# Performance work log

Hardware: AMD Instinct MI355X
Metric: run time of the kernel (lower is better)

## Reference

```python
import jax, jax.numpy as jnp
import numpy as np
from jax import lax

B, L, D, H, DH, NL, FF, V, CH = 64, 512, 384, 12, 32, 6, 1536, 30522, 64


def setup_inputs() -> dict:
    key = jax.random.key(0)
    ks = jax.random.split(key, 16)
    n = lambda i, shape, s: jax.random.normal(ks[i], shape, dtype=jnp.float32) * s
    return {
        "input_ids": jax.random.randint(ks[0], (B, L), 0, V),
        "attention_mask": jnp.ones((B, L), jnp.int32),
        "word_emb": n(1, (V, D), 0.02),
        "pos_emb": n(2, (L, D), 0.02),
        "type_emb": n(3, (2, D), 0.02),
        "emb_ln_w": jnp.ones((D,)), "emb_ln_b": jnp.zeros((D,)),
        "qW": n(4, (NL, D, D), 0.05), "kW": n(5, (NL, D, D), 0.05),
        "vW": n(6, (NL, D, D), 0.05), "oW": n(7, (NL, D, D), 0.05),
        "gW": n(8, (NL, D, D), 0.05),
        "convW": n(9, (NL, D, 1, 4), 0.1), "convB": jnp.zeros((NL, D)),
        "fdecay": jnp.full((NL, H, DH), 0.3, jnp.float32),
        "sdecay": jnp.full((NL, H, DH), 0.9, jnp.float32),
        "surW": n(10, (NL, 1, 2 * DH), 0.1), "surB": jnp.zeros((NL, 1)),
        "alpha": jnp.full((NL,), 0.5, jnp.float32),
        "ln1_w": jnp.ones((NL, D)), "ln1_b": jnp.zeros((NL, D)),
        "ffnW1": n(11, (NL, FF, D), 0.05), "ffnB1": jnp.zeros((NL, FF)),
        "ffnW2": n(12, (NL, D, FF), 0.05), "ffnB2": jnp.zeros((NL, D)),
        "ln2_w": jnp.ones((NL, D)), "ln2_b": jnp.zeros((NL, D)),
    }


def _ln(x, w, b, eps=1e-12):
    m = x.mean(-1, keepdims=True)
    v = ((x - m) ** 2).mean(-1, keepdims=True)
    return (x - m) * lax.rsqrt(v + eps) * w + b


def _delta(q, k, v, wfac):
    # chunked delta-rule linear attention: state[d,e] decays by wfac per chunk
    Bq, Hq, Lq, Dh = q.shape
    nC = Lq // CH
    chunk = lambda t: t.reshape(Bq, Hq, nC, CH, Dh).transpose(2, 0, 1, 3, 4)

    def step(state, xs):
        qc, kc, vc = xs
        state = state * wfac + jnp.einsum('bhld,bhle->bhde', vc, kc)
        return state, jnp.einsum('bhld,bhde->bhle', qc, state)

    s0 = jnp.zeros((Bq, Hq, Dh, Dh), q.dtype)
    _, o = lax.scan(step, s0, (chunk(q), chunk(k), chunk(v)))
    return o.transpose(1, 2, 0, 3, 4).reshape(Bq, Hq, Lq, Dh)


def _titan(x, qW, kW, vW, oW, gW, convW, convB, fdec, sdec, surW, surB, alpha):
    Bx, Lx, Dx = x.shape
    # depthwise conv1d, kernel=4, padding=2, truncate to L (torch semantics)
    xc = lax.conv_general_dilated(x.transpose(0, 2, 1), convW, (1,), [(2, 2)],
                                  feature_group_count=Dx,
                                  dimension_numbers=('NCH', 'OIH', 'NCH'))
    xc = (xc + convB[None, :, None])[:, :, :Lx].transpose(0, 2, 1)
    xc = jax.nn.silu(xc)
    proj = lambda W: (xc @ W.T).reshape(Bx, Lx, H, DH).transpose(0, 2, 1, 3)
    q, k, v = proj(qW), proj(kW), proj(vW)
    v = v * jax.nn.sigmoid(proj(gW))
    # surprise gate on concatenated (k, v)
    s = jax.nn.sigmoid((jnp.concatenate([k, v], -1) @ surW.T + surB) * 10.0)
    wfac_f = jnp.mean(jax.nn.sigmoid(fdec)) ** CH
    wfac_s = jnp.mean(jax.nn.sigmoid(sdec)) ** CH
    o_fast = _delta(q, k, v, wfac_f)
    o_slow = _delta(q, k * s, v * s, wfac_s)
    a = jax.nn.sigmoid(alpha)
    o = a * o_fast + (1.0 - a) * o_slow
    return o.transpose(0, 2, 1, 3).reshape(Bx, Lx, Dx) @ oW.T


def reference(input_ids, attention_mask, word_emb, pos_emb, type_emb, emb_ln_w,
              emb_ln_b, qW, kW, vW, oW, gW, convW, convB, fdecay, sdecay, surW,
              surB, alpha, ln1_w, ln1_b, ffnW1, ffnB1, ffnW2, ffnB2, ln2_w, ln2_b):
    x = word_emb[input_ids] + pos_emb[None, :L] + type_emb[0]
    x = _ln(x, emb_ln_w, emb_ln_b)
    for i in range(NL):
        attn = _titan(x, qW[i], kW[i], vW[i], oW[i], gW[i], convW[i], convB[i],
                      fdecay[i], sdecay[i], surW[i], surB[i], alpha[i])
        x = _ln(x + attn, ln1_w[i], ln1_b[i])
        h = jax.nn.gelu(x @ ffnW1[i].T + ffnB1[i], approximate=False)
        x = _ln(x + h @ ffnW2[i].T + ffnB2[i], ln2_w[i], ln2_b[i])
    m = attention_mask[..., None].astype(x.dtype)
    emb = (x * m).sum(1) / jnp.clip(m.sum(1), 1e-9)
    return emb / jnp.clip(jnp.linalg.norm(emb, axis=1, keepdims=True), 1e-12)
```

## Files before the change

### kernel.cpp

```cpp
#include <hip/hip_runtime.h>
#include <hip/hip_bf16.h>
#include <math.h>

constexpr int B_  = 64;
constexpr int L_  = 512;
constexpr int D_  = 384;
constexpr int H_  = 12;
constexpr int DH_ = 32;
constexpr int NL_ = 6;
constexpr int FF_ = 1536;
constexpr int CH_ = 64;
constexpr int MT  = B_ * L_;
constexpr int DD  = D_ * D_;

typedef float f32x4 __attribute__((ext_vector_type(4)));
typedef short s16x8 __attribute__((ext_vector_type(8)));
typedef short s16x4 __attribute__((ext_vector_type(4)));

__device__ __forceinline__ short f2bf(float f) {
    unsigned u = __float_as_uint(f);
    unsigned r = (u + 0x7fffu + ((u >> 16) & 1u)) >> 16;
    return (short)r;
}
__device__ __forceinline__ float bf2f(short s) {
    unsigned u = ((unsigned)(unsigned short)s) << 16;
    return __uint_as_float(u);
}

__global__ void cvt_kernel(const float* __restrict__ src, short* __restrict__ dst, int n8) {
    int i = blockIdx.x * 256 + threadIdx.x;
    if (i >= n8) return;
    const float4 lo = *(const float4*)(src + (size_t)i * 8);
    const float4 hi = *(const float4*)(src + (size_t)i * 8 + 4);
    s16x8 t;
    t[0] = f2bf(lo.x); t[1] = f2bf(lo.y); t[2] = f2bf(lo.z); t[3] = f2bf(lo.w);
    t[4] = f2bf(hi.x); t[5] = f2bf(hi.y); t[6] = f2bf(hi.z); t[7] = f2bf(hi.w);
    *(s16x8*)(dst + (size_t)i * 8) = t;
}

__global__ void cvt4_kernel(const float* __restrict__ q, const float* __restrict__ k,
                            const float* __restrict__ v, const float* __restrict__ g,
                            short* __restrict__ dst) {
    int i = blockIdx.x * 256 + threadIdx.x;
    if (i >= NL_ * DD / 8) return;
    const int l = i / (DD / 8), r = i - l * (DD / 8);
    const float* srcs[4] = {q, k, v, g};
#pragma unroll
    for (int w = 0; w < 4; w++) {
        const float4 lo = *(const float4*)(srcs[w] + (size_t)i * 8);
        const float4 hi = *(const float4*)(srcs[w] + (size_t)i * 8 + 4);
        s16x8 t;
        t[0] = f2bf(lo.x); t[1] = f2bf(lo.y); t[2] = f2bf(lo.z); t[3] = f2bf(lo.w);
        t[4] = f2bf(hi.x); t[5] = f2bf(hi.y); t[6] = f2bf(hi.z); t[7] = f2bf(hi.w);
        *(s16x8*)(dst + ((size_t)(l * 4 + w) * DD) + (size_t)r * 8) = t;
    }
}

__global__ __launch_bounds__(256) void embed_ln_kernel(
        const int* __restrict__ ids, const float* __restrict__ wemb,
        const float* __restrict__ pemb, const float* __restrict__ temb,
        const float* __restrict__ w, const float* __restrict__ b,
        float* __restrict__ out, short* __restrict__ outb) {
    const int t    = blockIdx.x * 4 + (threadIdx.x >> 6);
    const int lane = threadIdx.x & 63;
    const int l    = t % L_;
    const size_t ro = (size_t)t * D_;
    const size_t wo = (size_t)ids[t] * D_;
    const size_t po = (size_t)l * D_;

    float v[6];
    float s = 0.f;
#pragma unroll
    for (int j = 0; j < 6; j++) {
        const int d = j * 64 + lane;
        v[j] = wemb[wo + d] + pemb[po + d] + temb[d];
        s += v[j];
    }
#pragma unroll
    for (int o = 32; o > 0; o >>= 1) s += __shfl_xor(s, o);
    const float m = s * (1.f / D_);
    float s2 = 0.f;
#pragma unroll
    for (int j = 0; j < 6; j++) { v[j] -= m; s2 += v[j] * v[j]; }
#pragma unroll
    for (int o = 32; o > 0; o >>= 1) s2 += __shfl_xor(s2, o);
    const float r = rsqrtf(s2 * (1.f / D_) + 1e-12f);
#pragma unroll
    for (int j = 0; j < 6; j++) {
        const int d = j * 64 + lane;
        const float o = v[j] * r * w[d] + b[d];
        out[ro + d]  = o;
        outb[ro + d] = f2bf(o);
    }
}

__global__ __launch_bounds__(256) void ln_res_kernel(
        const short* __restrict__ y, float* __restrict__ x, short* __restrict__ xb,
        const float* __restrict__ w, const float* __restrict__ b) {
    const int t    = blockIdx.x * 4 + (threadIdx.x >> 6);
    const int lane = threadIdx.x & 63;
    const size_t ro = (size_t)t * D_;

    float v[6];
    float s = 0.f;
#pragma unroll
    for (int j = 0; j < 6; j++) {
        const int d = j * 64 + lane;
        v[j] = x[ro + d] + bf2f(y[ro + d]);
        s += v[j];
    }
#pragma unroll
    for (int o = 32; o > 0; o >>= 1) s += __shfl_xor(s, o);
    const float m = s * (1.f / D_);
    float s2 = 0.f;
#pragma unroll
    for (int j = 0; j < 6; j++) { v[j] -= m; s2 += v[j] * v[j]; }
#pragma unroll
    for (int o = 32; o > 0; o >>= 1) s2 += __shfl_xor(s2, o);
    const float r = rsqrtf(s2 * (1.f / D_) + 1e-12f);
#pragma unroll
    for (int j = 0; j < 6; j++) {
        const int d = j * 64 + lane;
        const float o = v[j] * r * w[d] + b[d];
        x[ro + d]  = o;
        xb[ro + d] = f2bf(o);
    }
}

__global__ void wfac_kernel(const float* __restrict__ fdec, const float* __restrict__ sdec,
                            float* __restrict__ wf) {
    const int l     = blockIdx.x >> 1;
    const int which = blockIdx.x & 1;
    const float* p  = (which ? sdec : fdec) + (size_t)l * H_ * DH_;
    float v = 1.f / (1.f + expf(-p[threadIdx.x]));
    __shared__ float red[6];
#pragma unroll
    for (int o = 32; o > 0; o >>= 1) v += __shfl_down(v, o);
    if ((threadIdx.x & 63) == 0) red[threadIdx.x >> 6] = v;
    __syncthreads();
    if (threadIdx.x == 0) {
        float s = 0.f;
        for (int i = 0; i < 6; i++) s += red[i];
        float m = s / (float)(H_ * DH_);
        for (int i = 0; i < 6; i++) m = m * m;
        wf[l * 2 + which] = m;
    }
}

__global__ __launch_bounds__(256) void conv_silu_kernel(
        const short* __restrict__ xb, const float* __restrict__ cw,
        const float* __restrict__ cb, short* __restrict__ out) {
    const int i8 = blockIdx.x * 256 + threadIdx.x;
    const int d8 = (i8 * 8) % D_;
    const int bl = (i8 * 8) / D_;
    const int l  = bl % L_;

    float acc[8];
#pragma unroll
    for (int jj = 0; jj < 8; jj++) acc[jj] = cb[d8 + jj];

    const short* xrow = xb + (size_t)(bl - l) * D_ + d8;
#pragma unroll
    for (int j = 0; j < 4; j++) {
        const int t = l + j - 2;
        if (t >= 0 && t < L_) {
            const s16x8 xv = *(const s16x8*)(xrow + (size_t)t * D_);
#pragma unroll
            for (int jj = 0; jj < 8; jj++)
                acc[jj] = fmaf(bf2f(xv[jj]), cw[(d8 + jj) * 4 + j], acc[jj]);
        }
    }
    s16x8 o;
#pragma unroll
    for (int jj = 0; jj < 8; jj++) {
        const float sv = acc[jj] / (1.f + expf(-acc[jj]));
        o[jj] = f2bf(sv);
    }
    *(s16x8*)(out + (size_t)i8 * 8) = o;
}

template <int ACT, bool BIAS>
__global__ __launch_bounds__(256) void gemm_mfma(const short* __restrict__ A_b,
                                                 const short* __restrict__ Wb,
                                                 const float* __restrict__ bias,
                                                 short* __restrict__ Cb0,
                                                 int N, int K, int zsW, int zsC) {
    const short* W = Wb + (size_t)blockIdx.z * zsW;

    __shared__ short As[2][4096];
    __shared__ short Ws[2][4096];

    const int bm = blockIdx.y * 128, bn = blockIdx.x * 128;
    const int tid = threadIdx.x;
    const int wv = tid >> 6, lane = tid & 63;
    const int wr = wv >> 1, wc = wv & 1;
    const int l16 = lane & 15, kqr = lane >> 4;
    (void)wv; (void)lane;

    int srow[2], sq[2], sslot[2];
#pragma unroll
    for (int i = 0; i < 2; i++) {
        const int c = tid + i * 256;
        const int r = c >> 2;
        const int q = c & 3;
        srow[i]  = r;
        sq[i]    = q;
        sslot[i] = r * 4 + (q ^ ((r ^ (r >> 2)) & 3));
    }

    f32x4 acc[4][4];
    const f32x4 zr = {0.f, 0.f, 0.f, 0.f};
#pragma unroll
    for (int i = 0; i < 4; i++)
#pragma unroll
        for (int j = 0; j < 4; j++) acc[i][j] = zr;

    const int NT = K >> 5;
    s16x8 ra[2], rw[2];

#pragma unroll
    for (int i = 0; i < 2; i++) {
        ra[i] = *(const s16x8*)(A_b + (size_t)(bm + srow[i]) * K + sq[i] * 8);
        rw[i] = *(const s16x8*)(W   + (size_t)(bn + srow[i]) * K + sq[i] * 8);
    }
#pragma unroll
    for (int i = 0; i < 2; i++) {
        *(s16x8*)&As[0][sslot[i] * 8] = ra[i];
        *(s16x8*)&Ws[0][sslot[i] * 8] = rw[i];
    }
    __syncthreads();

    for (int kt = 0; kt < NT; ++kt) {
        const int buf = kt & 1;
        if (kt + 1 < NT) {
            const int ko = (kt + 1) * 32;
#pragma unroll
            for (int i = 0; i < 2; i++) {
                ra[i] = *(const s16x8*)(A_b + (size_t)(bm + srow[i]) * K + ko + sq[i] * 8);
                rw[i] = *(const s16x8*)(W   + (size_t)(bn + srow[i]) * K + ko + sq[i] * 8);
            }
        }

        s16x8 af[4], bf[4];
#pragma unroll
        for (int i = 0; i < 4; i++) {
            const int r = wr * 64 + i * 16 + l16;
            const int slot = r * 4 + (kqr ^ ((r ^ (r >> 2)) & 3));
            af[i] = *(const s16x8*)&As[buf][slot * 8];
        }
#pragma unroll
        for (int j = 0; j < 4; j++) {
            const int r = wc * 64 + j * 16 + l16;
            const int slot = r * 4 + (kqr ^ ((r ^ (r >> 2)) & 3));
            bf[j] = *(const s16x8*)&Ws[buf][slot * 8];
        }
#pragma unroll
        for (int i = 0; i < 4; i++)
#pragma unroll
            for (int j = 0; j < 4; j++)
                acc[i][j] = __builtin_amdgcn_mfma_f32_16x16x32_bf16(af[i], bf[j], acc[i][j], 0, 0, 0);

        if (kt + 1 < NT) {
            __syncthreads();
#pragma unroll
            for (int i = 0; i < 2; i++) {
                *(s16x8*)&As[buf ^ 1][sslot[i] * 8] = ra[i];
                *(s16x8*)&Ws[buf ^ 1][sslot[i] * 8] = rw[i];
            }
        }
        __syncthreads();
    }

    short* Cb = Cb0 + (size_t)blockIdx.z * zsC;
#pragma unroll
    for (int i = 0; i < 4; i++) {
        const int m0 = bm + wr * 64 + i * 16 + kqr * 4;
#pragma unroll
        for (int j = 0; j < 4; j++) {
            const int n = bn + wc * 64 + j * 16 + l16;
            float bv = 0.f;
            if (BIAS) bv = bias[n];
            const f32x4 v = acc[i][j];
#pragma unroll
            for (int r = 0; r < 4; r++) {
                float o = v[r] + bv;
                if (ACT == 1) o = 0.5f * o * (1.f + erff(o * 0.70710678118654752f));
                Cb[(size_t)(m0 + r) * N + n] = f2bf(o);
            }
        }
    }
}

__global__ __launch_bounds__(256) void delta_kernel(const short* __restrict__ qb,
                                                    const short* __restrict__ kb,
                                                    const short* __restrict__ vb,
                                                    const short* __restrict__ gb,
                                                    const float* __restrict__ surW,
                                                    const float* __restrict__ surB,
                                                    const float* __restrict__ wf,
                                                    const float* __restrict__ alpha,
                                                    int layer, short* __restrict__ ob) {
    const int bh = blockIdx.x;
    const int b = bh / H_, h = bh % H_;
    const int tid = threadIdx.x;
    const float wfa = wf[layer * 2 + 0], wsa = wf[layer * 2 + 1];
    const float a = 1.f / (1.f + expf(-alpha[layer]));
    const float sbias = surB[0];

    __shared__ float qS[CH_][36], kS[CH_][36], vS[CH_][36];
    __shared__ float s2S[CH_];
    __shared__ float Sc[DH_][36];
    __shared__ float swS[64];

    if (tid < 64) swS[tid] = surW[tid];
    __syncthreads();

    const int d  = tid >> 3;
    const int e4 = (tid & 7) * 4;
    const int lo = tid >> 2;
    const int e8 = (tid & 3) * 8;

    float sf[4] = {0.f, 0.f, 0.f, 0.f};
    float ss[4] = {0.f, 0.f, 0.f, 0.f};

    const size_t base = ((size_t)b * L_) * D_ + (size_t)h * DH_;

    for (int c = 0; c < L_ / CH_; c++) {
        const int l0 = c * CH_;
#pragma unroll
        for (int i = 0; i < 2; i++) {
            const int c4 = tid + i * 256;
            const int ll = c4 >> 3, dd4 = (c4 & 7) * 4;
            const size_t g = base + (size_t)(l0 + ll) * D_ + dd4;
            const s16x4 q4 = *(const s16x4*)(qb + g);
            const s16x4 k4 = *(const s16x4*)(kb + g);
            const s16x4 v4 = *(const s16x4*)(vb + g);
            const s16x4 g4 = *(const s16x4*)(gb + g);
            float p = 0.f;
#pragma unroll
            for (int j = 0; j < 4; j++) {
                const float kf = bf2f(k4[j]);
                const float gv = bf2f(g4[j]);
                const float vg = bf2f(v4[j]) / (1.f + expf(-gv));
                qS[ll][dd4 + j] = bf2f(q4[j]);
                kS[ll][dd4 + j] = kf;
                vS[ll][dd4 + j] = vg;
                p += kf * swS[dd4 + j] + vg * swS[32 + dd4 + j];
            }
            p += __shfl_xor(p, 1);
            p += __shfl_xor(p, 2);
            p += __shfl_xor(p, 4);
            if ((tid & 7) == 0) {
                const float sv = 1.f / (1.f + expf(-10.f * (p + sbias)));
                s2S[ll] = sv * sv;
            }
        }
        __syncthreads();

#pragma unroll
        for (int j = 0; j < 4; j++) { sf[j] *= wfa; ss[j] *= wsa; }
        for (int l = 0; l < CH_; l++) {
            const float vd = vS[l][d];
            const float s2 = s2S[l];
            const float4 k4 = *(const float4*)&kS[l][e4];
            const float kk[4] = {k4.x, k4.y, k4.z, k4.w};
#pragma unroll
            for (int j = 0; j < 4; j++) {
                const float p = vd * kk[j];
                sf[j] += p;
                ss[j] = fmaf(p, s2, ss[j]);
            }
        }
        float4 scv;
        scv.x = a * sf[0] + (1.f - a) * ss[0];
        scv.y = a * sf[1] + (1.f - a) * ss[1];
        scv.z = a * sf[2] + (1.f - a) * ss[2];
        scv.w = a * sf[3] + (1.f - a) * ss[3];
        *(float4*)&Sc[d][e4] = scv;
        __syncthreads();

        float o8[8] = {0.f, 0.f, 0.f, 0.f, 0.f, 0.f, 0.f, 0.f};
        for (int dd = 0; dd < DH_; dd++) {
            const float qv = qS[lo][dd];
            const float4 s0 = *(const float4*)&Sc[dd][e8];
            const float4 s1 = *(const float4*)&Sc[dd][e8 + 4];
            o8[0] = fmaf(qv, s0.x, o8[0]); o8[1] = fmaf(qv, s0.y, o8[1]);
            o8[2] = fmaf(qv, s0.z, o8[2]); o8[3] = fmaf(qv, s0.w, o8[3]);
            o8[4] = fmaf(qv, s1.x, o8[4]); o8[5] = fmaf(qv, s1.y, o8[5]);
            o8[6] = fmaf(qv, s1.z, o8[6]); o8[7] = fmaf(qv, s1.w, o8[7]);
        }
        s16x8 t;
#pragma unroll
        for (int j = 0; j < 8; j++) t[j] = f2bf(o8[j]);
        *(s16x8*)(ob + base + (size_t)(l0 + lo) * D_ + e8) = t;
        __syncthreads();
    }
}

__global__ __launch_bounds__(384) void pool_partial_kernel(
        const float* __restrict__ x, const int* __restrict__ mask,
        float* __restrict__ partial, float* __restrict__ maskp) {
    const int b  = blockIdx.x >> 3;
    const int ch = blockIdx.x & 7;
    const int dd = threadIdx.x;
    const int lb = ch * 64;
    float sum = 0.f;
    for (int l = 0; l < 64; l++) {
        const float m = (float)mask[b * L_ + lb + l];
        sum = fmaf(x[((size_t)(b * L_ + lb + l)) * D_ + dd], m, sum);
    }
    partial[(size_t)blockIdx.x * D_ + dd] = sum;
    if (dd < 64) {
        float mm = (float)mask[b * L_ + lb + dd];
#pragma unroll
        for (int o = 32; o > 0; o >>= 1) mm += __shfl_xor(mm, o);
        if (dd == 0) maskp[blockIdx.x] = mm;
    }
}

__global__ __launch_bounds__(384) void pool_finalize_kernel(
        const float* __restrict__ partial, const float* __restrict__ maskp,
        float* __restrict__ out) {
    const int b  = blockIdx.x;
    const int dd = threadIdx.x;
    float sum = 0.f, msum = 0.f;
#pragma unroll
    for (int c = 0; c < 8; c++) {
        sum  += partial[(size_t)(b * 8 + c) * D_ + dd];
        msum += maskp[b * 8 + c];
    }
    const float emb = sum / fmaxf(msum, 1e-9f);

    __shared__ float red[6];
    __shared__ float scale;
    float q = emb * emb;
#pragma unroll
    for (int o = 32; o > 0; o >>= 1) q += __shfl_down(q, o);
    if ((dd & 63) == 0) red[dd >> 6] = q;
    __syncthreads();
    if (dd == 0) {
        float t = 0.f;
        for (int i = 0; i < 6; i++) t += red[i];
        scale = 1.f / fmaxf(sqrtf(t), 1e-12f);
    }
    __syncthreads();
    out[(size_t)b * D_ + dd] = emb * scale;
}

extern "C" void kernel_launch(void* const* d_in, const int* in_sizes, int n_in,
                              void* d_out, int out_size, void* d_ws, size_t ws_size,
                              hipStream_t stream) {
    (void)in_sizes; (void)n_in; (void)out_size; (void)ws_size;

    const int*   ids   = (const int*)d_in[0];
    const int*   mask  = (const int*)d_in[1];
    const float* wemb  = (const float*)d_in[2];
    const float* pemb  = (const float*)d_in[3];
    const float* temb  = (const float*)d_in[4];
    const float* elnw  = (const float*)d_in[5];
    const float* elnb  = (const float*)d_in[6];
    const float* qW    = (const float*)d_in[7];
    const float* kW    = (const float*)d_in[8];
    const float* vW    = (const float*)d_in[9];
    const float* oW    = (const float*)d_in[10];
    const float* gW    = (const float*)d_in[11];
    const float* convW = (const float*)d_in[12];
    const float* convB = (const float*)d_in[13];
    const float* fdec  = (const float*)d_in[14];
    const float* sdec  = (const float*)d_in[15];
    const float* surW  = (const float*)d_in[16];
    const float* surB  = (const float*)d_in[17];
    const float* alpha = (const float*)d_in[18];
    const float* ln1w  = (const float*)d_in[19];
    const float* ln1b  = (const float*)d_in[20];
    const float* fW1   = (const float*)d_in[21];
    const float* fB1   = (const float*)d_in[22];
    const float* fW2   = (const float*)d_in[23];
    const float* fB2   = (const float*)d_in[24];
    const float* ln2w  = (const float*)d_in[25];
    const float* ln2b  = (const float*)d_in[26];

    float* x     = (float*)d_ws;
    float* wfp   = x + (size_t)MT * D_;
    float* pp    = wfp + 16;
    float* mp    = pp + (size_t)B_ * 8 * D_;
    short* qkvg  = (short*)(mp + B_ * 8);
    short* xb    = qkvg + (size_t)4 * MT * D_;
    short* xcb   = xb + (size_t)MT * D_;
    short* wqkvg = xcb + (size_t)MT * D_;
    short* wo    = wqkvg + (size_t)NL_ * 4 * DD;
    short* wf1   = wo + (size_t)NL_ * DD;
    short* wf2   = wf1 + (size_t)NL_ * FF_ * D_;

    short* q16 = qkvg;
    short* k16 = q16 + (size_t)MT * D_;
    short* v16 = k16 + (size_t)MT * D_;
    short* g16 = v16 + (size_t)MT * D_;
    short* attn = qkvg;
    short* hb   = qkvg;
    short* dob  = xcb;

    cvt4_kernel<<<NL_ * DD / 8 / 256, 256, 0, stream>>>(qW, kW, vW, gW, wqkvg);
    cvt_kernel<<<NL_ * DD / 8 / 256, 256, 0, stream>>>(oW, wo, NL_ * DD / 8);
    cvt_kernel<<<NL_ * FF_ * D_ / 8 / 256, 256, 0, stream>>>(fW1, wf1, NL_ * FF_ * D_ / 8);
    cvt_kernel<<<NL_ * FF_ * D_ / 8 / 256, 256, 0, stream>>>(fW2, wf2, NL_ * FF_ * D_ / 8);

    embed_ln_kernel<<<MT / 4, 256, 0, stream>>>(ids, wemb, pemb, temb, elnw, elnb, x, xb);
    wfac_kernel<<<NL_ * 2, 384, 0, stream>>>(fdec, sdec, wfp);

    const dim3 g1(D_ / 128, MT / 128, 1);
    const dim3 g2(FF_ / 128, MT / 128, 1);
    const dim3 gq(D_ / 128, MT / 128, 4);

    for (int i = 0; i < NL_; i++) {
        conv_silu_kernel<<<(MT * D_ / 8) / 256, 256, 0, stream>>>(
            xb, convW + (size_t)i * D_ * 4, convB + (size_t)i * D_, xcb);

        gemm_mfma<0, false><<<gq, 256, 0, stream>>>(
            xcb, wqkvg + (size_t)i * 4 * DD, nullptr, qkvg, D_, D_, DD, MT * D_);

        delta_kernel<<<B_ * H_, 256, 0, stream>>>(
            q16, k16, v16, g16, surW + (size_t)i * 2 * DH_, surB + i, wfp, alpha, i, dob);

        gemm_mfma<0, false><<<g1, 256, 0, stream>>>(
            dob, wo + (size_t)i * DD, nullptr, attn, D_, D_, 0, 0);
        ln_res_kernel<<<MT / 4, 256, 0, stream>>>(attn, x, xb, ln1w + (size_t)i * D_, ln1b + (size_t)i * D_);

        gemm_mfma<1, true><<<g2, 256, 0, stream>>>(
            xb, wf1 + (size_t)i * FF_ * D_, fB1 + (size_t)i * FF_, hb, FF_, D_, 0, 0);
        gemm_mfma<0, true><<<g1, 256, 0, stream>>>(
            hb, wf2 + (size_t)i * FF_ * D_, fB2 + (size_t)i * D_, xcb, D_, FF_, 0, 0);
        ln_res_kernel<<<MT / 4, 256, 0, stream>>>(xcb, x, xb, ln2w + (size_t)i * D_, ln2b + (size_t)i * D_);
    }

    pool_partial_kernel<<<B_ * 8, 384, 0, stream>>>(x, mask, pp, mp);
    pool_finalize_kernel<<<B_, 384, 0, stream>>>(pp, mp, (float*)d_out);
}
```

Measured before the change: 2.851 ms.

## Use direct global-to-LDS loads in GEMM and interleave QKVG output layout

The GEMM main loop now issues global_load_lds 16-byte transfers straight into the swizzled shared-memory buffers. This replaces the register staging and the extra barrier plus LDS store that came before. The Q/K/V/G projection becomes one GEMM with N=4*D writing a token-interleaved [MT,4D] buffer, and the delta kernel reads q/k/v/g from that layout at fixed offsets. The aim is to save register traffic and a sync per k-step. The cost is that the swizzled LDS slot mapping now depends on the wave/lane order of the direct-load writes, and the delta kernel's loads become strided across a wider row.

New measurement: 2.838 ms. Within noise of the previous version (-0.4%).

```diff
diff --git a/kernel.cpp b/kernel.cpp
--- a/kernel.cpp
+++ b/kernel.cpp
@@ -12,6 +12,7 @@
 constexpr int CH_ = 64;
 constexpr int MT  = B_ * L_;
 constexpr int DD  = D_ * D_;
+constexpr int TS  = 4 * D_;
 
 typedef float f32x4 __attribute__((ext_vector_type(4)));
 typedef short s16x8 __attribute__((ext_vector_type(8)));
@@ -25,6 +26,11 @@
 __device__ __forceinline__ float bf2f(short s) {
     unsigned u = ((unsigned)(unsigned short)s) << 16;
     return __uint_as_float(u);
+}
+
+__device__ __forceinline__ void gl_lds16(const void* g, void* l) {
+    __builtin_amdgcn_global_load_lds((const __attribute__((address_space(1))) void*)g,
+                                     (__attribute__((address_space(3))) void*)l, 16, 0, 0);
 }
 
 __global__ void cvt_kernel(const float* __restrict__ src, short* __restrict__ dst, int n8) {
@@ -181,12 +187,10 @@
 
 template <int ACT, bool BIAS>
 __global__ __launch_bounds__(256) void gemm_mfma(const short* __restrict__ A_b,
-                                                 const short* __restrict__ Wb,
+                                                 const short* __restrict__ W,
                                                  const float* __restrict__ bias,
-                                                 short* __restrict__ Cb0,
-                                                 int N, int K, int zsW, int zsC) {
-    const short* W = Wb + (size_t)blockIdx.z * zsW;
-
+                                                 short* __restrict__ Cb,
+                                                 int N, int K) {
     __shared__ short As[2][4096];
     __shared__ short Ws[2][4096];
 
@@ -195,17 +199,14 @@
     const int wv = tid >> 6, lane = tid & 63;
     const int wr = wv >> 1, wc = wv & 1;
     const int l16 = lane & 15, kqr = lane >> 4;
-    (void)wv; (void)lane;
-
-    int srow[2], sq[2], sslot[2];
+
+    int srow[2], skq[2];
 #pragma unroll
     for (int i = 0; i < 2; i++) {
         const int c = tid + i * 256;
         const int r = c >> 2;
-        const int q = c & 3;
-        srow[i]  = r;
-        sq[i]    = q;
-        sslot[i] = r * 4 + (q ^ ((r ^ (r >> 2)) & 3));
+        srow[i] = r;
+        skq[i] = (c & 3) ^ ((r ^ (r >> 2)) & 3);
     }
 
     f32x4 acc[4][4];
@@ -216,17 +217,13 @@
         for (int j = 0; j < 4; j++) acc[i][j] = zr;
 
     const int NT = K >> 5;
-    s16x8 ra[2], rw[2];
 
 #pragma unroll
     for (int i = 0; i < 2; i++) {
-        ra[i] = *(const s16x8*)(A_b + (size_t)(bm + srow[i]) * K + sq[i] * 8);
-        rw[i] = *(const s16x8*)(W   + (size_t)(bn + srow[i]) * K + sq[i] * 8);
-    }
-#pragma unroll
-    for (int i = 0; i < 2; i++) {
-        *(s16x8*)&As[0][sslot[i] * 8] = ra[i];
-        *(s16x8*)&Ws[0][sslot[i] * 8] = rw[i];
+        short* la = &As[0][(wv * 64 + i * 256) * 8];
+        short* lw = &Ws[0][(wv * 64 + i * 256) * 8];
+        gl_lds16(A_b + (size_t)(bm + srow[i]) * K + skq[i] * 8, la);
+        gl_lds16(W   + (size_t)(bn + srow[i]) * K + skq[i] * 8, lw);
     }
     __syncthreads();
 
@@ -236,8 +233,10 @@
             const int ko = (kt + 1) * 32;
 #pragma unroll
             for (int i = 0; i < 2; i++) {
-                ra[i] = *(const s16x8*)(A_b + (size_t)(bm + srow[i]) * K + ko + sq[i] * 8);
-                rw[i] = *(const s16x8*)(W   + (size_t)(bn + srow[i]) * K + ko + sq[i] * 8);
+                short* la = &As[buf ^ 1][(wv * 64 + i * 256) * 8];
+                short* lw = &Ws[buf ^ 1][(wv * 64 + i * 256) * 8];
+                gl_lds16(A_b + (size_t)(bm + srow[i]) * K + ko + skq[i] * 8, la);
+                gl_lds16(W   + (size_t)(bn + srow[i]) * K + ko + skq[i] * 8, lw);
             }
         }
 
@@ -260,18 +259,9 @@
             for (int j = 0; j < 4; j++)
                 acc[i][j] = __builtin_amdgcn_mfma_f32_16x16x32_bf16(af[i], bf[j], acc[i][j], 0, 0, 0);
 
-        if (kt + 1 < NT) {
-            __syncthreads();
-#pragma unroll
-            for (int i = 0; i < 2; i++) {
-                *(s16x8*)&As[buf ^ 1][sslot[i] * 8] = ra[i];
-                *(s16x8*)&Ws[buf ^ 1][sslot[i] * 8] = rw[i];
-            }
-        }
         __syncthreads();
     }
 
-    short* Cb = Cb0 + (size_t)blockIdx.z * zsC;
 #pragma unroll
     for (int i = 0; i < 4; i++) {
         const int m0 = bm + wr * 64 + i * 16 + kqr * 4;
@@ -291,10 +281,7 @@
     }
 }
 
-__global__ __launch_bounds__(256) void delta_kernel(const short* __restrict__ qb,
-                                                    const short* __restrict__ kb,
-                                                    const short* __restrict__ vb,
-                                                    const short* __restrict__ gb,
+__global__ __launch_bounds__(256) void delta_kernel(const short* __restrict__ qkvgb,
                                                     const float* __restrict__ surW,
                                                     const float* __restrict__ surB,
                                                     const float* __restrict__ wf,
@@ -323,7 +310,7 @@
     float sf[4] = {0.f, 0.f, 0.f, 0.f};
     float ss[4] = {0.f, 0.f, 0.f, 0.f};
 
-    const size_t base = ((size_t)b * L_) * D_ + (size_t)h * DH_;
+    const size_t obase = ((size_t)b * L_) * D_ + (size_t)h * DH_;
 
     for (int c = 0; c < L_ / CH_; c++) {
         const int l0 = c * CH_;
@@ -331,11 +318,11 @@
         for (int i = 0; i < 2; i++) {
             const int c4 = tid + i * 256;
             const int ll = c4 >> 3, dd4 = (c4 & 7) * 4;
-            const size_t g = base + (size_t)(l0 + ll) * D_ + dd4;
-            const s16x4 q4 = *(const s16x4*)(qb + g);
-            const s16x4 k4 = *(const s16x4*)(kb + g);
-            const s16x4 v4 = *(const s16x4*)(vb + g);
-            const s16x4 g4 = *(const s16x4*)(gb + g);
+            const size_t g = ((size_t)(b * L_) + l0 + ll) * TS + h * DH_ + dd4;
+            const s16x4 q4 = *(const s16x4*)(qkvgb + g);
+            const s16x4 k4 = *(const s16x4*)(qkvgb + g + D_);
+            const s16x4 v4 = *(const s16x4*)(qkvgb + g + 2 * D_);
+            const s16x4 g4 = *(const s16x4*)(qkvgb + g + 3 * D_);
             float p = 0.f;
 #pragma unroll
             for (int j = 0; j < 4; j++) {
@@ -392,7 +379,7 @@
         s16x8 t;
 #pragma unroll
         for (int j = 0; j < 8; j++) t[j] = f2bf(o8[j]);
-        *(s16x8*)(ob + base + (size_t)(l0 + lo) * D_ + e8) = t;
+        *(s16x8*)(ob + obase + (size_t)(l0 + lo) * D_ + e8) = t;
         __syncthreads();
     }
 }
@@ -485,17 +472,13 @@
     float* pp    = wfp + 16;
     float* mp    = pp + (size_t)B_ * 8 * D_;
     short* qkvg  = (short*)(mp + B_ * 8);
-    short* xb    = qkvg + (size_t)4 * MT * D_;
+    short* xb    = qkvg + (size_t)MT * TS;
     short* xcb   = xb + (size_t)MT * D_;
     short* wqkvg = xcb + (size_t)MT * D_;
     short* wo    = wqkvg + (size_t)NL_ * 4 * DD;
     short* wf1   = wo + (size_t)NL_ * DD;
     short* wf2   = wf1 + (size_t)NL_ * FF_ * D_;
 
-    short* q16 = qkvg;
-    short* k16 = q16 + (size_t)MT * D_;
-    short* v16 = k16 + (size_t)MT * D_;
-    short* g16 = v16 + (size_t)MT * D_;
     short* attn = qkvg;
     short* hb   = qkvg;
     short* dob  = xcb;
@@ -508,28 +491,27 @@
     embed_ln_kernel<<<MT / 4, 256, 0, stream>>>(ids, wemb, pemb, temb, elnw, elnb, x, xb);
     wfac_kernel<<<NL_ * 2, 384, 0, stream>>>(fdec, sdec, wfp);
 
-    const dim3 g1(D_ / 128, MT / 128, 1);
-    const dim3 g2(FF_ / 128, MT / 128, 1);
-    const dim3 gq(D_ / 128, MT / 128, 4);
+    const dim3 g1(D_ / 128, MT / 128);
+    const dim3 g2(FF_ / 128, MT / 128);
 
     for (int i = 0; i < NL_; i++) {
         conv_silu_kernel<<<(MT * D_ / 8) / 256, 256, 0, stream>>>(
             xb, convW + (size_t)i * D_ * 4, convB + (size_t)i * D_, xcb);
 
-        gemm_mfma<0, false><<<gq, 256, 0, stream>>>(
-            xcb, wqkvg + (size_t)i * 4 * DD, nullptr, qkvg, D_, D_, DD, MT * D_);
+        gemm_mfma<0, false><<<g2, 256, 0, stream>>>(
+            xcb, wqkvg + (size_t)i * 4 * DD, nullptr, qkvg, TS, D_);
 
         delta_kernel<<<B_ * H_, 256, 0, stream>>>(
-            q16, k16, v16, g16, surW + (size_t)i * 2 * DH_, surB + i, wfp, alpha, i, dob);
+            qkvg, surW + (size_t)i * 2 * DH_, surB + i, wfp, alpha, i, dob);
 
         gemm_mfma<0, false><<<g1, 256, 0, stream>>>(
-            dob, wo + (size_t)i * DD, nullptr, attn, D_, D_, 0, 0);
+            dob, wo + (size_t)i * DD, nullptr, attn, D_, D_);
         ln_res_kernel<<<MT / 4, 256, 0, stream>>>(attn, x, xb, ln1w + (size_t)i * D_, ln1b + (size_t)i * D_);
 
         gemm_mfma<1, true><<<g2, 256, 0, stream>>>(
-            xb, wf1 + (size_t)i * FF_ * D_, fB1 + (size_t)i * FF_, hb, FF_, D_, 0, 0);
+            xb, wf1 + (size_t)i * FF_ * D_, fB1 + (size_t)i * FF_, hb, FF_, D_);
         gemm_mfma<0, true><<<g1, 256, 0, stream>>>(
-            hb, wf2 + (size_t)i * FF_ * D_, fB2 + (size_t)i * D_, xcb, D_, FF_, 0, 0);
+            hb, wf2 + (size_t)i * FF_ * D_, fB2 + (size_t)i * D_, xcb, D_, FF_);
         ln_res_kernel<<<MT / 4, 256, 0, stream>>>(xcb, x, xb, ln2w + (size_t)i * D_, ln2b + (size_t)i * D_);
     }
 
```
